# Performance work log

Hardware: AMD Instinct MI355X
Metric: run time of the kernel (lower is better)

## Reference

```python
import jax, jax.numpy as jnp
import numpy as np
from jax.scipy.linalg import solve_triangular

OMEGA0 = 30.0  # standard SIREN first-layer frequency


def setup_inputs() -> dict:
    key = jax.random.key(0)
    ks = jax.random.split(key, 12)
    B, NC, NT, XD, H, R = 64, 1024, 1024, 1, 512, 512
    x_context = jax.random.normal(ks[0], (B, NC, XD), jnp.float32)
    y_context = jax.random.normal(ks[1], (B, NC, 1), jnp.float32)
    x_target = jax.random.normal(ks[2], (B, NT, XD), jnp.float32)
    # SIREN MLP params (hidden_dims=[512,512,512], repr_dim=512)
    def lin(k, fi, fo, first=False):
        bound = 1.0 / fi if first else np.sqrt(6.0 / fi) / OMEGA0
        kW, kb = jax.random.split(k)
        W = jax.random.uniform(kW, (fi, fo), jnp.float32, -bound, bound)
        b = jax.random.uniform(kb, (fo,), jnp.float32, -bound, bound)
        return W, b
    W0, b0 = lin(ks[3], XD, H, first=True)
    W1, b1 = lin(ks[4], H, H)
    W2, b2 = lin(ks[5], H, H)
    Wr, br = lin(ks[6], H, R)
    log_noise_var = jnp.asarray(np.log(0.01), jnp.float32)
    return {"x_context": x_context, "y_context": y_context, "x_target": x_target,
            "W0": W0, "b0": b0, "W1": W1, "b1": b1, "W2": W2, "b2": b2,
            "Wr": Wr, "br": br, "log_noise_var": log_noise_var}


def _mlp(x, W0, b0, W1, b1, W2, b2, Wr, br):
    # SIREN: sine activations, omega_0 on first layer, linear head
    h = jnp.sin(OMEGA0 * (x @ W0 + b0))
    h = jnp.sin(h @ W1 + b1)
    h = jnp.sin(h @ W2 + b2)
    return h @ Wr + br


def reference(x_context, y_context, x_target, W0, b0, W1, b1, W2, b2, Wr, br, log_noise_var):
    mean = jnp.mean(y_context, axis=1, keepdims=True)          # [B,1,1]
    std = jnp.std(y_context, axis=1, keepdims=True, ddof=1)    # torch.std is unbiased
    yc = (y_context - mean) / std                              # [B,N,1]

    cr = _mlp(x_context, W0, b0, W1, b1, W2, b2, Wr, br)       # [B,N,R]
    tr = _mlp(x_target, W0, b0, W1, b1, W2, b2, Wr, br)        # [B,M,R]
    ones_c = jnp.ones(cr.shape[:-1] + (1,), cr.dtype)
    ones_t = jnp.ones(tr.shape[:-1] + (1,), tr.dtype)
    cr = jnp.concatenate([cr, ones_c], axis=-1)                # [B,N,R+1]
    tr = jnp.concatenate([tr, ones_t], axis=-1)                # [B,M,R+1]

    Rp1 = cr.shape[-1]
    cov = jnp.einsum('bnr,bns->brs', cr, cr)                   # [B,R+1,R+1]
    cov = cov + jnp.exp(log_noise_var) * jnp.eye(Rp1, dtype=cov.dtype)
    xty = jnp.einsum('bnr,bnd->brd', cr, yc)                   # [B,R+1,1]

    chol = jnp.linalg.cholesky(cov)                            # batched potrf
    z = solve_triangular(chol, xty, lower=True)
    w = solve_triangular(jnp.swapaxes(chol, -1, -2), z, lower=False)  # [B,R+1,1]

    y_pred = tr @ w                                            # [B,M,1]
    return y_pred * std + mean
```

## Files before the change

kernel.cpp:

```cpp
#include <hip/hip_runtime.h>
#include <hip/hip_fp16.h>
#include <math.h>

#define NB    64
#define NPTS  1024
#define HD    512
#define CPAD  576
#define COVE  ((size_t)NB*CPAD*CPAD)

typedef __attribute__((ext_vector_type(4))) float v4f;
typedef __attribute__((ext_vector_type(8))) short v8s;
typedef __attribute__((ext_vector_type(8))) _Float16 v8h;

__device__ __forceinline__ float sin_poly(float z){
  float t = z*z;
  float p = fmaf(t, -1.9841270e-4f, 8.3333333e-3f);
  p = fmaf(t, p, -0.16666667f);
  p = fmaf(t, p, 1.0f);
  return z*p;
}

__device__ __forceinline__ ushort2 split_f16(float a){
  _Float16 h = (_Float16)a;
  float hf = (float)h;
  _Float16 l = (_Float16)(a - hf);
  unsigned short uh, ul;
  __builtin_memcpy(&uh, &h, 2);
  __builtin_memcpy(&ul, &l, 2);
  ushort2 r; r.x = uh; r.y = ul;
  return r;
}

__device__ __forceinline__ unsigned short f16b(float a){
  _Float16 h = (_Float16)a;
  unsigned short uh; __builtin_memcpy(&uh, &h, 2);
  return uh;
}

__device__ __forceinline__ float f16r(float a){
  return (float)(_Float16)a;
}

__device__ __forceinline__ void g2l16(const unsigned short* g, unsigned short* l){
  __builtin_amdgcn_global_load_lds(
      (const __attribute__((address_space(1))) unsigned int*)(g),
      (__attribute__((address_space(3))) unsigned int*)(l), 16, 0, 0);
}

__global__ __launch_bounds__(256)
void prep_k(const float* __restrict__ W1, const float* __restrict__ W2,
            const float* __restrict__ Wr, unsigned short* __restrict__ wf,
            const float* __restrict__ y, float* __restrict__ meanv,
            float* __restrict__ stdv, float* __restrict__ ycb)
{
  __shared__ unsigned short tile[64][65];
  __shared__ float rs[4], rss[4], bc[2];
  const int tid = threadIdx.x;
  if (blockIdx.x >= 192){
    const int b = blockIdx.x - 192;
    const float* yb = y + (size_t)b*NPTS;
    float4 v = *(const float4*)(yb + tid*4);
    float s  = v.x+v.y+v.z+v.w;
    float ss = v.x*v.x+v.y*v.y+v.z*v.z+v.w*v.w;
    #pragma unroll
    for (int off=32; off; off>>=1){ s += __shfl_down(s, off); ss += __shfl_down(ss, off); }
    int wid = tid>>6, lane = tid&63;
    if (lane == 0){ rs[wid]=s; rss[wid]=ss; }
    __syncthreads();
    if (tid == 0){
      float S  = rs[0]+rs[1]+rs[2]+rs[3];
      float SS = rss[0]+rss[1]+rss[2]+rss[3];
      float mean = S * (1.0f/NPTS);
      float var  = (SS - S*S*(1.0f/NPTS)) * (1.0f/(NPTS-1));
      float sd = sqrtf(var);
      meanv[b]=mean; stdv[b]=sd; bc[0]=mean; bc[1]=1.0f/sd;
    }
    __syncthreads();
    float mean=bc[0], inv=bc[1];
    float4 o;
    o.x=(v.x-mean)*inv; o.y=(v.y-mean)*inv; o.z=(v.z-mean)*inv; o.w=(v.w-mean)*inv;
    *(float4*)(ycb + (size_t)b*NPTS + tid*4) = o;
    return;
  }
  const int mat = blockIdx.x >> 6;
  const int t = blockIdx.x & 63;
  const int k0 = (t >> 3)*64, n0 = (t & 7)*64;
  const float* W = (mat==0) ? W1 : ((mat==1) ? W2 : Wr);
  for (int idx=tid; idx<4096; idx+=256){
    int r = idx >> 6, c = idx & 63;
    tile[r][c] = f16b(W[(size_t)(k0+r)*512 + n0 + c]);
  }
  __syncthreads();
  unsigned short* dst = wf + (size_t)mat*262144;
  for (int idx=tid; idx<4096; idx+=256){
    int r = idx >> 6, c = idx & 63;
    dst[(size_t)(n0+r)*512 + k0 + c] = tile[c][r];
  }
}

__device__ __forceinline__ void h0c(const float* __restrict__ w0,
                                    const float* __restrict__ b0, int K0, int sq,
                                    float xv0, float xv1, v8s& pa0, v8s& pa1)
{
  const float* wp = w0 + K0 + sq*8;
  const float* bp = b0 + K0 + sq*8;
  float4 wva = *(const float4*)wp, wvb = *(const float4*)(wp+4);
  float4 bva = *(const float4*)bp, bvb = *(const float4*)(bp+4);
  float w8[8] = {wva.x,wva.y,wva.z,wva.w,wvb.x,wvb.y,wvb.z,wvb.w};
  float b8[8] = {bva.x,bva.y,bva.z,bva.w,bvb.x,bvb.y,bvb.z,bvb.w};
  #pragma unroll
  for (int i=0;i<8;++i){
    pa0[i] = (short)f16b(__sinf(30.f*fmaf(xv0, w8[i], b8[i])));
    pa1[i] = (short)f16b(__sinf(30.f*fmaf(xv1, w8[i], b8[i])));
  }
}

template<int EPI, int TRANS, int AMODE>
__global__ __launch_bounds__(256, 2)
void gemm_ld(const unsigned short* __restrict__ Ap,
             const float* __restrict__ xsrc, const float* __restrict__ w0,
             const float* __restrict__ b0,
             const unsigned short* __restrict__ Bw,
             const float* __restrict__ bias,
             unsigned short* __restrict__ Chi, unsigned short* __restrict__ Clo,
             const float* __restrict__ vvp, float* __restrict__ ydot, int rowBase)
{
  __shared__ unsigned short Ah[2][4096], Bh[2][8192];
  const int tid  = threadIdx.x;
  const int lane = tid & 63, wave = tid >> 6;
  const int wm = wave & 1, wn = wave >> 1;
  const int m0 = blockIdx.x*128, n0 = blockIdx.y*256;
  const int q = lane >> 4, ln16 = lane & 15;
  const int sr = tid >> 2, sq = tid & 3;
  const int qx  = (q ^ ((ln16>>1)&3))*8;
  const int swc = ((lane&3) ^ ((lane>>3)&3))*8;
  const int wsl = (sq ^ ((sr>>1)&3))*8;

  const int strowA = wave*32 + (lane>>2);
  const int strowB = wave*64 + (lane>>2);
  const unsigned short* gA = Ap + (size_t)(m0 + strowA)*512 + swc;
  const unsigned short* gB = Bw + (size_t)(n0 + strowB)*512 + swc;

  float xv0 = 0.f, xv1 = 0.f;
  if (AMODE == 1){ xv0 = xsrc[m0 + sr]; xv1 = xsrc[m0 + sr + 64]; }

  v4f acc[4][8];
  #pragma unroll
  for (int a=0;a<4;++a)
    #pragma unroll
    for (int b=0;b<8;++b) acc[a][b] = (v4f)(0.0f);

  v8s pa0, pa1;
  if (AMODE == 0){
    g2l16(gA, Ah[0]+wave*1024); g2l16(gA+16*512, Ah[0]+wave*1024+512);
  } else {
    h0c(w0, b0, 0, sq, xv0, xv1, pa0, pa1);
    *(v8s*)(Ah[0] + sr*32 + wsl) = pa0;
    *(v8s*)(Ah[0] + (sr+64)*32 + wsl) = pa1;
  }
  #pragma unroll
  for (int m=0;m<4;++m) g2l16(gB + m*16*512, Bh[0]+wave*2048 + m*512);
  __syncthreads();

  int cur = 0;
  for (int ks=0; ks<16; ++ks){
    const int nxt = cur^1;
    if (ks < 15){
      const int k1 = (ks+1)*32;
      if (AMODE == 0){
        g2l16(gA+k1, Ah[nxt]+wave*1024); g2l16(gA+k1+16*512, Ah[nxt]+wave*1024+512);
      }
      #pragma unroll
      for (int m=0;m<4;++m) g2l16(gB + k1 + m*16*512, Bh[nxt]+wave*2048 + m*512);
    }
    v8h bhf[8];
    #pragma unroll
    for (int nt=0; nt<8; ++nt){
      const int nrow = wn*128 + nt*16 + ln16;
      bhf[nt] = *(const v8h*)(Bh[cur] + nrow*32 + qx);
    }
    #pragma unroll
    for (int mt=0; mt<4; ++mt){
      const int mrow = wm*64 + mt*16 + ln16;
      v8h ah = *(const v8h*)(Ah[cur] + mrow*32 + qx);
      #pragma unroll
      for (int nt=0; nt<8; ++nt)
        acc[mt][nt] = __builtin_amdgcn_mfma_f32_16x16x32_f16(ah, bhf[nt], acc[mt][nt], 0,0,0);
    }
    if (AMODE == 1 && ks < 15){
      h0c(w0, b0, (ks+1)*32, sq, xv0, xv1, pa0, pa1);
      *(v8s*)(Ah[nxt] + sr*32 + wsl) = pa0;
      *(v8s*)(Ah[nxt] + (sr+64)*32 + wsl) = pa1;
    }
    __syncthreads();
    cur = nxt;
  }

  if (TRANS == 0){
    #pragma unroll
    for (int nt=0;nt<8;++nt){
      const int col = n0 + wn*128 + nt*16 + ln16;
      const float bl_ = bias[col];
      #pragma unroll
      for (int mt=0;mt<4;++mt){
        const int row0 = m0 + wm*64 + mt*16 + q*4;
        #pragma unroll
        for (int r=0;r<4;++r){
          float v = acc[mt][nt][r] + bl_;
          if (EPI == 1) v = sin_poly(v);
          Chi[(size_t)(row0+r)*512 + col] = f16b(v);
        }
      }
    }
  } else if (TRANS == 1){
    const int lb = m0 >> 10;
    #pragma unroll
    for (int nt=0;nt<8;++nt){
      const int col = n0 + wn*128 + nt*16 + ln16;
      const float bl_ = bias[col];
      #pragma unroll
      for (int mt=0;mt<4;++mt){
        const int row0 = m0 + wm*64 + mt*16 + q*4;
        const int nb = row0 & 1023;
        ushort4 h,l; ushort2 s;
        s=split_f16(acc[mt][nt][0]+bl_); h.x=s.x; l.x=s.y;
        s=split_f16(acc[mt][nt][1]+bl_); h.y=s.x; l.y=s.y;
        s=split_f16(acc[mt][nt][2]+bl_); h.z=s.x; l.z=s.y;
        s=split_f16(acc[mt][nt][3]+bl_); h.w=s.x; l.w=s.y;
        size_t o = ((size_t)lb*512 + col)*1024 + nb;
        *(ushort4*)(Chi + o) = h;
        *(ushort4*)(Clo + o) = l;
      }
    }
  } else {
    const int b = (rowBase + m0) >> 10;
    const float* vb = vvp + (size_t)b*512;
    float vcol[8];
    float bl_[8];
    #pragma unroll
    for (int nt=0;nt<8;++nt){
      const int col = n0 + wn*128 + nt*16 + ln16;
      vcol[nt] = vb[col];
      bl_[nt] = bias[col];
    }
    #pragma unroll
    for (int mt=0;mt<4;++mt){
      #pragma unroll
      for (int r=0;r<4;++r){
        float part = 0.f;
        #pragma unroll
        for (int nt=0;nt<8;++nt)
          part = fmaf(sin_poly(acc[mt][nt][r] + bl_[nt]), vcol[nt], part);
        #pragma unroll
        for (int off=1; off<16; off<<=1) part += __shfl_xor(part, off, 64);
        if (ln16 == 0){
          const int row = m0 + wm*64 + mt*16 + q*4 + r;
          atomicAdd(&ydot[rowBase + row], part);
        }
      }
    }
  }
}

__device__ __forceinline__ void ld_ext_row(const unsigned short* __restrict__ h,
                                           const unsigned short* __restrict__ l,
                                           const float* __restrict__ ycn,
                                           int f, int nofs, v8s& oh, v8s& ol)
{
  if (f < 512){
    oh = *(const v8s*)(h + (size_t)f*1024 + nofs);
    ol = *(const v8s*)(l + (size_t)f*1024 + nofs);
  } else if (f == 512){
    #pragma unroll
    for (int j=0;j<8;++j){ oh[j] = (short)0x3C00; ol[j] = 0; }
  } else if (f == 513){
    #pragma unroll
    for (int j=0;j<8;++j){
      ushort2 s = split_f16(ycn[nofs+j]);
      oh[j] = (short)s.x; ol[j] = (short)s.y;
    }
  } else {
    #pragma unroll
    for (int j=0;j<8;++j){ oh[j] = 0; ol[j] = 0; }
  }
}

__global__ __launch_bounds__(256)
void cov_ld(const unsigned short* __restrict__ CThi, const unsigned short* __restrict__ CTlo,
            const float* __restrict__ ycb,
            const float* __restrict__ lnv, float* __restrict__ cov, int bStart)
{
  int t = blockIdx.y;
  int ti = 0;
  while ((ti+1)*(ti+2)/2 <= t) ++ti;
  int tj = t - ti*(ti+1)/2;
  const int i0 = ti*128, j0 = tj*128;
  const int lb = blockIdx.x;
  const int b  = bStart + lb;
  const unsigned short* srch = CThi + (size_t)lb*512*1024;
  const unsigned short* srcl = CTlo + (size_t)lb*512*1024;
  const float* ycn = ycb + (size_t)b*NPTS;
  float* covb = cov + (size_t)b*CPAD*CPAD;
  const float noise = expf(lnv[0]);
  const bool diag = (i0 == j0);
  const bool aReg = (i0 == 512);

  __shared__ unsigned short Ah[2][4096], Al[2][4096], Bh2[2][4096], Bl2[2][4096];
  const int tid = threadIdx.x;
  const int lane = tid & 63, wave = tid >> 6;
  const int wm = wave & 1, wn = wave >> 1;
  const int q = lane >> 4, ln16 = lane & 15;
  const int sr = tid >> 2, sq = tid & 3;
  const int qx  = (q ^ ((ln16>>1)&3))*8;
  const int swc = ((lane&3) ^ ((lane>>3)&3))*8;
  const int wsl = (sq ^ ((sr>>1)&3))*8;
  const bool skipW = diag && (wave == 2);

  const int strow = wave*32 + (lane>>2);
  const size_t gaOff = (size_t)(i0 + strow)*1024 + swc;
  const size_t gbOff = (size_t)(j0 + strow)*1024 + swc;
  const int wb = wave*1024;

  v4f acc[4][4];
  #pragma unroll
  for (int a=0;a<4;++a)
    #pragma unroll
    for (int c=0;c<4;++c) acc[a][c] = (v4f)(0.0f);

  if (!aReg){
    g2l16(srch + gaOff, Ah[0]+wb); g2l16(srch + gaOff + (size_t)16*1024, Ah[0]+wb+512);
    g2l16(srcl + gaOff, Al[0]+wb); g2l16(srcl + gaOff + (size_t)16*1024, Al[0]+wb+512);
  } else {
    v8s th, tl;
    ld_ext_row(srch, srcl, ycn, i0 + sr, sq*8, th, tl);
    *(v8s*)(Ah[0] + sr*32 + wsl) = th; *(v8s*)(Al[0] + sr*32 + wsl) = tl;
    ld_ext_row(srch, srcl, ycn, i0 + sr + 64, sq*8, th, tl);
    *(v8s*)(Ah[0] + (sr+64)*32 + wsl) = th; *(v8s*)(Al[0] + (sr+64)*32 + wsl) = tl;
  }
  if (!diag){
    g2l16(srch + gbOff, Bh2[0]+wb); g2l16(srch + gbOff + (size_t)16*1024, Bh2[0]+wb+512);
    g2l16(srcl + gbOff, Bl2[0]+wb); g2l16(srcl + gbOff + (size_t)16*1024, Bl2[0]+wb+512);
  }
  __syncthreads();

  int cur = 0;
  for (int ks=0; ks<32; ++ks){
    const int nxt = cur^1;
    if (ks < 31){
      const int k1 = (ks+1)*32;
      if (!aReg){
        g2l16(srch + gaOff + k1, Ah[nxt]+wb);
        g2l16(srch + gaOff + k1 + (size_t)16*1024, Ah[nxt]+wb+512);
        g2l16(srcl + gaOff + k1, Al[nxt]+wb);
        g2l16(srcl + gaOff + k1 + (size_t)16*1024, Al[nxt]+wb+512);
      }
      if (!diag){
        g2l16(srch + gbOff + k1, Bh2[nxt]+wb);
        g2l16(srch + gbOff + k1 + (size_t)16*1024, Bh2[nxt]+wb+512);
        g2l16(srcl + gbOff + k1, Bl2[nxt]+wb);
        g2l16(srcl + gbOff + k1 + (size_t)16*1024, Bl2[nxt]+wb+512);
      }
    }
    if (!skipW){
      const unsigned short* BhP = diag ? Ah[cur] : Bh2[cur];
      const unsigned short* BlP = diag ? Al[cur] : Bl2[cur];
      v8h bhf[4], blf[4];
      #pragma unroll
      for (int nt=0; nt<4; ++nt){
        const int nrow = wn*64 + nt*16 + ln16;
        bhf[nt] = *(const v8h*)(BhP + nrow*32 + qx);
        blf[nt] = *(const v8h*)(BlP + nrow*32 + qx);
      }
      #pragma unroll
      for (int mt=0; mt<4; ++mt){
        const int mrow = wm*64 + mt*16 + ln16;
        v8h ah = *(const v8h*)(Ah[cur] + mrow*32 + qx);
        v8h al = *(const v8h*)(Al[cur] + mrow*32 + qx);
        #pragma unroll
        for (int nt=0; nt<4; ++nt){
          acc[mt][nt] = __builtin_amdgcn_mfma_f32_16x16x32_f16(ah, bhf[nt], acc[mt][nt], 0,0,0);
          acc[mt][nt] = __builtin_amdgcn_mfma_f32_16x16x32_f16(ah, blf[nt], acc[mt][nt], 0,0,0);
          acc[mt][nt] = __builtin_amdgcn_mfma_f32_16x16x32_f16(al, bhf[nt], acc[mt][nt], 0,0,0);
        }
      }
    }
    if (aReg && ks < 31){
      const int n1 = (ks+1)*32 + sq*8;
      v8s th, tl;
      ld_ext_row(srch, srcl, ycn, i0 + sr, n1, th, tl);
      *(v8s*)(Ah[nxt] + sr*32 + wsl) = th; *(v8s*)(Al[nxt] + sr*32 + wsl) = tl;
      ld_ext_row(srch, srcl, ycn, i0 + sr + 64, n1, th, tl);
      *(v8s*)(Ah[nxt] + (sr+64)*32 + wsl) = th; *(v8s*)(Al[nxt] + (sr+64)*32 + wsl) = tl;
    }
    __syncthreads();
    cur = nxt;
  }
  #pragma unroll
  for (int nt=0;nt<4;++nt){
    const int gj = j0 + wn*64 + nt*16 + ln16;
    #pragma unroll
    for (int mt=0;mt<4;++mt){
      const int gi0 = i0 + wm*64 + mt*16 + q*4;
      #pragma unroll
      for (int r=0;r<4;++r){
        const int gi = gi0 + r;
        if (gj <= gi && gi < CPAD && gj < CPAD){
          float v = acc[mt][nt][r];
          if (gi == gj) v += (gi < 513) ? noise : 1.0f;
          covb[(size_t)gi*CPAD + gj] = v;
        }
      }
    }
  }
}

__global__ __launch_bounds__(256)
void chol_trsm_k(float* __restrict__ cov, float* __restrict__ dchol, int k)
{
  (void)dchol;
  float* Ab = cov + (size_t)blockIdx.x * CPAD * CPAD;
  const int o = k*64;
  const int row0 = o + 64 + blockIdx.y*128;
  const int nrows = min(128, CPAD - row0);
  __shared__ float Ds[64][65];
  __shared__ float As[128][65];
  __shared__ float invd[64];
  const int tid = threadIdx.x;

  for (int idx=tid; idx<nrows*16; idx+=256){
    int r = idx >> 4, c = (idx & 15)*4;
    float4 v = *(const float4*)(Ab + (size_t)(row0+r)*CPAD + o + c);
    As[r][c]=v.x; As[r][c+1]=v.y; As[r][c+2]=v.z; As[r][c+3]=v.w;
  }

  if (tid < 64){
    float a[64];
    const float* rowp = Ab + (size_t)(o+tid)*CPAD + o;
    #pragma unroll
    for (int c=0; c<64; c+=4){
      float4 v = *(const float4*)(rowp + c);
      a[c]   = (c   <= tid) ? v.x : 0.f;
      a[c+1] = (c+1 <= tid) ? v.y : 0.f;
      a[c+2] = (c+2 <= tid) ? v.z : 0.f;
      a[c+3] = (c+3 <= tid) ? v.w : 0.f;
    }
    #pragma unroll
    for (int j=0; j<63; ++j){
      float vj = a[j];
      float t = vj * (1.0f / __shfl(vj, j, 64));
      #pragma unroll
      for (int c=j+1; c<64; ++c)
        a[c] = fmaf(-t, __shfl(vj, c, 64), a[c]);
    }
    float myinv = 0.f;
    #pragma unroll
    for (int c=0; c<64; ++c){
      float ic = 1.0f / sqrtf(__shfl(a[c], c, 64));
      a[c] *= ic;
      myinv = (c == tid) ? ic : myinv;
    }
    invd[tid] = myinv;
    #pragma unroll
    for (int c=0; c<64; ++c) Ds[tid][c] = a[c];
  }
  __syncthreads();

  const int srow = tid - 64;
  if (srow >= 0 && srow < nrows){
    float x[64];
    #pragma unroll
    for (int c=0; c<64; ++c){
      float s0 = As[srow][c], s1 = 0.f, s2 = 0.f, s3 = 0.f;
      #pragma unroll
      for (int j=0; j+4<=c; j+=4){
        s0 = fmaf(-x[j],   Ds[c][j],   s0);
        s1 = fmaf(-x[j+1], Ds[c][j+1], s1);
        s2 = fmaf(-x[j+2], Ds[c][j+2], s2);
        s3 = fmaf(-x[j+3], Ds[c][j+3], s3);
      }
      #pragma unroll
      for (int j = c & ~3; j < c; ++j)
        s0 = fmaf(-x[j], Ds[c][j], s0);
      x[c] = ((s0+s1)+(s2+s3)) * invd[c];
    }
    #pragma unroll
    for (int c=0; c<64; ++c) As[srow][c] = x[c];
  } else if (blockIdx.y == 0 && tid >= 192){
    const int r = tid - 192;
    float y[64];
    #pragma unroll
    for (int c = 63; c >= 0; --c){
      float s0 = (c == r) ? 1.0f : 0.0f, s1 = 0.f, s2 = 0.f, s3 = 0.f;
      #pragma unroll
      for (int j = c+1; j+4 <= 64; j += 4){
        s0 = fmaf(-Ds[j][c],   y[j],   s0);
        s1 = fmaf(-Ds[j+1][c], y[j+1], s1);
        s2 = fmaf(-Ds[j+2][c], y[j+2], s2);
        s3 = fmaf(-Ds[j+3][c], y[j+3], s3);
      }
      #pragma unroll
      for (int j = c+1 + ((63-c) & ~3); j < 64; ++j)
        s0 = fmaf(-Ds[j][c], y[j], s0);
      y[c] = ((s0+s1)+(s2+s3)) * invd[c];
    }
    float* dst = Ab + (size_t)(o + r)*CPAD + 512;
    #pragma unroll
    for (int c = 0; c < 64; c += 4)
      *(float4*)(dst + c) = make_float4(y[c], y[c+1], y[c+2], y[c+3]);
  }
  __syncthreads();
  for (int idx=tid; idx<nrows*16; idx+=256){
    int r = idx >> 4, c = (idx & 15)*4;
    float4 v = make_float4(As[r][c], As[r][c+1], As[r][c+2], As[r][c+3]);
    *(float4*)(Ab + (size_t)(row0+r)*CPAD + o + c) = v;
  }
}

__global__ __launch_bounds__(256)
void chol_trail_k(float* __restrict__ cov, int k)
{
  float* Ab = cov + (size_t)blockIdx.y * CPAD * CPAD;
  int t = blockIdx.x;
  int bi = 0;
  while ((bi+1)*(bi+2)/2 <= t) ++bi;
  int bj = t - bi*(bi+1)/2;
  const int o = k*64;
  const int s0 = o + 64;
  const int I = s0 + bi*64, J = s0 + bj*64;
  const bool diag = (bi == bj);

  __shared__ unsigned short Pih[64*72], Pil[64*72], Pjh[64*72], Pjl[64*72];
  const int tid = threadIdx.x;
  const int lane = tid & 63, wave = tid >> 6;
  const int q = lane >> 4, ln16 = lane & 15;

  for (int idx=tid; idx<1024; idx+=256){
    int r = idx >> 4, c = (idx & 15)*4;
    float4 v = *(const float4*)(Ab + (size_t)(I+r)*CPAD + o + c);
    ushort4 hh, ll; ushort2 s;
    s=split_f16(v.x); hh.x=s.x; ll.x=s.y;
    s=split_f16(v.y); hh.y=s.x; ll.y=s.y;
    s=split_f16(v.z); hh.z=s.x; ll.z=s.y;
    s=split_f16(v.w); hh.w=s.x; ll.w=s.y;
    *(ushort4*)(Pih + r*72 + c) = hh;
    *(ushort4*)(Pil + r*72 + c) = ll;
    if (!diag){
      float4 u = *(const float4*)(Ab + (size_t)(J+r)*CPAD + o + c);
      s=split_f16(u.x); hh.x=s.x; ll.x=s.y;
      s=split_f16(u.y); hh.y=s.x; ll.y=s.y;
      s=split_f16(u.z); hh.z=s.x; ll.z=s.y;
      s=split_f16(u.w); hh.w=s.x; ll.w=s.y;
      *(ushort4*)(Pjh + r*72 + c) = hh;
      *(ushort4*)(Pjl + r*72 + c) = ll;
    }
  }
  __syncthreads();
  const unsigned short* Bh = diag ? Pih : Pjh;
  const unsigned short* Bl = diag ? Pil : Pjl;

  v4f acc[4];
  #pragma unroll
  for (int nt=0;nt<4;++nt) acc[nt] = (v4f)(0.0f);

  #pragma unroll
  for (int ks=0; ks<2; ++ks){
    const int ko = ks*32 + q*8;
    v8h ah = *(const v8h*)(Pih + (wave*16 + ln16)*72 + ko);
    v8h al = *(const v8h*)(Pil + (wave*16 + ln16)*72 + ko);
    #pragma unroll
    for (int nt=0; nt<4; ++nt){
      v8h bh = *(const v8h*)(Bh + (nt*16 + ln16)*72 + ko);
      v8h bl = *(const v8h*)(Bl + (nt*16 + ln16)*72 + ko);
      acc[nt] = __builtin_amdgcn_mfma_f32_16x16x32_f16(ah, bh, acc[nt], 0,0,0);
      acc[nt] = __builtin_amdgcn_mfma_f32_16x16x32_f16(ah, bl, acc[nt], 0,0,0);
      acc[nt] = __builtin_amdgcn_mfma_f32_16x16x32_f16(al, bh, acc[nt], 0,0,0);
    }
  }

  #pragma unroll
  for (int nt=0; nt<4; ++nt){
    const int gj = J + nt*16 + ln16;
    #pragma unroll
    for (int r=0; r<4; ++r){
      const int gi = I + wave*16 + q*4 + r;
      if (gj <= gi)
        Ab[(size_t)gi*CPAD + gj] -= acc[nt][r];
    }
  }
}

__global__ __launch_bounds__(256)
void chol_last_k(float* __restrict__ cov, float* __restrict__ dchol)
{
  float* Ab = cov + (size_t)blockIdx.x * CPAD * CPAD;
  __shared__ float P[64][65];
  __shared__ float Ds[64][65];
  __shared__ float invl[64];
  const int tid = threadIdx.x;

  for (int idx=tid; idx<1024; idx+=256){
    int r = idx >> 4, c = (idx & 15)*4;
    float4 v = *(const float4*)(Ab + (size_t)(512+r)*CPAD + 448 + c);
    P[r][c]=v.x; P[r][c+1]=v.y; P[r][c+2]=v.z; P[r][c+3]=v.w;
    float4 u = *(const float4*)(Ab + (size_t)(512+r)*CPAD + 512 + c);
    Ds[r][c]   = (c   <= r) ? u.x : 0.f;
    Ds[r][c+1] = (c+1 <= r) ? u.y : 0.f;
    Ds[r][c+2] = (c+2 <= r) ? u.z : 0.f;
    Ds[r][c+3] = (c+3 <= r) ? u.w : 0.f;
  }
  __syncthreads();
  {
    const int tx = tid & 15, ty = tid >> 4;
    float acc[4][4];
    #pragma unroll
    for (int r=0;r<4;++r)
      #pragma unroll
      for (int c=0;c<4;++c) acc[r][c]=0.f;
    for (int kk=0; kk<64; ++kk){
      float av[4], bv[4];
      #pragma unroll
      for (int r=0;r<4;++r) av[r] = P[tx*4+r][kk];
      #pragma unroll
      for (int c=0;c<4;++c) bv[c] = P[ty*4+c][kk];
      #pragma unroll
      for (int r=0;r<4;++r)
        #pragma unroll
        for (int c=0;c<4;++c) acc[r][c] = fmaf(av[r], bv[c], acc[r][c]);
    }
    __syncthreads();
    #pragma unroll
    for (int r=0;r<4;++r){
      int gi = tx*4 + r;
      #pragma unroll
      for (int c=0;c<4;++c){
        int gj = ty*4 + c;
        if (gj <= gi) Ds[gi][gj] -= acc[r][c];
      }
    }
  }
  __syncthreads();

  if (tid < 64){
    float a[64];
    #pragma unroll
    for (int c=0; c<64; ++c) a[c] = Ds[tid][c];
    #pragma unroll
    for (int j=0; j<63; ++j){
      float vj = a[j];
      float t = vj * (1.0f / __shfl(vj, j, 64));
      #pragma unroll
      for (int c=j+1; c<64; ++c)
        a[c] = fmaf(-t, __shfl(vj, c, 64), a[c]);
    }
    float myinv = 0.f;
    #pragma unroll
    for (int c=0; c<64; ++c){
      float ic = 1.0f / sqrtf(__shfl(a[c], c, 64));
      a[c] *= ic;
      myinv = (c == tid) ? ic : myinv;
    }
    invl[tid] = myinv;
    #pragma unroll
    for (int c=0; c<64; ++c) Ds[tid][c] = a[c];
  }
  __syncthreads();

  float* dst = dchol + ((size_t)blockIdx.x*9 + 8)*4096;
  for (int idx=tid; idx<4096; idx+=256)
    dst[idx] = Ds[idx>>6][idx&63];
  if (tid < 64){
    const int r = tid;
    float y[64];
    #pragma unroll
    for (int c = 63; c >= 0; --c){
      float s0 = (c == r) ? 1.0f : 0.0f, s1 = 0.f, s2 = 0.f, s3 = 0.f;
      #pragma unroll
      for (int j = c+1; j+4 <= 64; j += 4){
        s0 = fmaf(-Ds[j][c],   y[j],   s0);
        s1 = fmaf(-Ds[j+1][c], y[j+1], s1);
        s2 = fmaf(-Ds[j+2][c], y[j+2], s2);
        s3 = fmaf(-Ds[j+3][c], y[j+3], s3);
      }
      #pragma unroll
      for (int j = c+1 + ((63-c) & ~3); j < 64; ++j)
        s0 = fmaf(-Ds[j][c], y[j], s0);
      y[c] = ((s0+s1)+(s2+s3)) * invl[c];
    }
    float* dst2 = Ab + (size_t)(512 + r)*CPAD + 512;
    #pragma unroll
    for (int c = 0; c < 64; c += 4)
      *(float4*)(dst2 + c) = make_float4(y[c], y[c+1], y[c+2], y[c+3]);
  }
}

__global__ __launch_bounds__(1024)
void back_solve_k(const float* __restrict__ cov, const float* __restrict__ dchol,
                  const float* __restrict__ Wr, const float* __restrict__ br,
                  float* __restrict__ vv, float* __restrict__ cvec,
                  float* __restrict__ ydot)
{
  const int b = blockIdx.x;
  const float* L = cov + (size_t)b*CPAD*CPAD;
  const float* dc = dchol + (size_t)b*9*4096;
  __shared__ float inv2[64*64];
  __shared__ float rhs[CPAD];
  __shared__ float xv[64];
  __shared__ float red[4*512];
  const int tid = threadIdx.x;
  const int pr = tid >> 4, pc = (tid & 15)*4;
  const float* zrow = L + (size_t)513*CPAD;

  for (int i=tid; i<CPAD; i+=1024)
    rhs[i] = (i < 512) ? zrow[i] : ((i == 512) ? dc[8*4096 + 64] : 0.f);
  {
    float4 v = *(const float4*)(L + (size_t)(512 + pr)*CPAD + 512 + pc);
    *(float4*)(inv2 + pr*64 + pc) = v;
  }
  __syncthreads();

  for (int k=8; k>=1; --k){
    const int o = k*64;
    const int G = o >> 2;
    const int act = G << 2;
    float4 v16[16];
    int rg = 0, cg = 0;
    if (tid < act){
      rg = tid / G; cg = tid % G;
      const float* lp = L + (size_t)(o + rg*16)*CPAD + cg*4;
      #pragma unroll
      for (int rr=0; rr<16; ++rr)
        v16[rr] = *(const float4*)(lp + (size_t)rr*CPAD);
    }
    float4 pf = *(const float4*)(L + (size_t)((k-1)*64 + pr)*CPAD + 512 + pc);
    if (tid < 64){
      float acc = 0.f;
      #pragma unroll
      for (int j=0;j<64;++j) acc = fmaf(inv2[j*64 + tid], rhs[o+j], acc);
      xv[tid] = acc;
      rhs[o+tid] = acc;
    }
    __syncthreads();
    if (tid < act){
      float4 s = {0.f,0.f,0.f,0.f};
      #pragma unroll
      for (int rr=0; rr<16; ++rr){
        float xr = xv[rg*16 + rr];
        s.x = fmaf(v16[rr].x, xr, s.x);
        s.y = fmaf(v16[rr].y, xr, s.y);
        s.z = fmaf(v16[rr].z, xr, s.z);
        s.w = fmaf(v16[rr].w, xr, s.w);
      }
      *(float4*)(red + rg*512 + cg*4) = s;
    }
    __syncthreads();
    if (tid < o)
      rhs[tid] -= (red[tid] + red[512+tid]) + (red[1024+tid] + red[1536+tid]);
    *(float4*)(inv2 + pr*64 + pc) = pf;
    __syncthreads();
  }
  if (tid < 64){
    float acc = 0.f;
    #pragma unroll
    for (int j=0;j<64;++j) acc = fmaf(inv2[j*64 + tid], rhs[j], acc);
    rhs[tid] = acc;
  }
  __syncthreads();

  ydot[(size_t)b*1024 + tid] = 0.f;
  const int j = tid >> 1, h = tid & 1;
  {
    float acc = 0.f;
    const float* row = Wr + (size_t)j*512 + h*256;
    const float* wsp = rhs + h*256;
    for (int r=0; r<256; r+=4){
      float4 w4 = *(const float4*)(row + r);
      acc = fmaf(f16r(w4.x), wsp[r],   acc);
      acc = fmaf(f16r(w4.y), wsp[r+1], acc);
      acc = fmaf(f16r(w4.z), wsp[r+2], acc);
      acc = fmaf(f16r(w4.w), wsp[r+3], acc);
    }
    red[tid] = acc;
  }
  __syncthreads();
  if (h == 0) vv[(size_t)b*512 + j] = red[tid] + red[tid+1];
  __syncthreads();
  red[tid] = (tid < 512) ? br[tid]*rhs[tid] : 0.f;
  __syncthreads();
  for (int s2=512; s2>0; s2>>=1){
    if (tid < s2) red[tid] += red[tid+s2];
    __syncthreads();
  }
  if (tid == 0) cvec[b] = red[0] + rhs[512];
}

__global__ __launch_bounds__(256)
void fin_k(const float* __restrict__ ydot, const float* __restrict__ cvec,
           const float* __restrict__ meanv, const float* __restrict__ stdv,
           float* __restrict__ out)
{
  int i = blockIdx.x*256 + threadIdx.x;
  int b = i >> 10;
  out[i] = fmaf(ydot[i] + cvec[b], stdv[b], meanv[b]);
}

extern "C" void kernel_launch(void* const* d_in, const int* in_sizes, int n_in,
                              void* d_out, int out_size, void* d_ws, size_t ws_size,
                              hipStream_t stream)
{
  (void)in_sizes; (void)n_in; (void)out_size;
  const float* x_ctx = (const float*)d_in[0];
  const float* y_ctx = (const float*)d_in[1];
  const float* x_tgt = (const float*)d_in[2];
  const float* W0 = (const float*)d_in[3];
  const float* b0 = (const float*)d_in[4];
  const float* W1 = (const float*)d_in[5];
  const float* b1 = (const float*)d_in[6];
  const float* W2 = (const float*)d_in[7];
  const float* b2 = (const float*)d_in[8];
  const float* Wr = (const float*)d_in[9];
  const float* br = (const float*)d_in[10];
  const float* lnv = (const float*)d_in[11];
  float* out = (float*)d_out;
  float* ws = (float*)d_ws;

  int CH = 65536;
  for (;;){
    size_t fl = COVE + 65536 + 192 + (size_t)64*512 + (size_t)64*CPAD + 65536
              + (size_t)64*9*4096 + 64;
    size_t sh = (size_t)3*262144 + (size_t)2*CH*512 + (size_t)2*(CH/1024)*512*1024;
    size_t need = fl*4 + sh*2;
    if (ws_size >= need || CH <= 1024) break;
    CH >>= 1;
  }
  const int nch = 65536 / CH;
  const int bpc = CH / NPTS;

  float* cov   = ws;
  float* ycb   = cov + COVE;
  float* meanv = ycb + 65536;
  float* stdv  = meanv + 64;
  float* cvec  = stdv + 64;
  float* vvb   = cvec + 64;
  float* wvb   = vvb + (size_t)64*512;
  float* ydot  = wvb + (size_t)64*CPAD;
  float* dchol = ydot + 65536;
  unsigned short* wf   = (unsigned short*)(dchol + (size_t)64*9*4096);
  unsigned short* P0   = wf + (size_t)3*262144;
  unsigned short* P1   = P0 + (size_t)CH*512;
  unsigned short* CThi = P1 + (size_t)CH*512;
  unsigned short* CTlo = CThi + (size_t)bpc*512*1024;

  prep_k<<<256, 256, 0, stream>>>(W1, W2, Wr, wf, y_ctx, meanv, stdv, ycb);

  for (int c=0; c<nch; ++c){
    const float* xc = x_ctx + (size_t)c*CH;
    dim3 g(CH/128, 2);
    gemm_ld<1,0,1><<<g, 256, 0, stream>>>(0, xc, W0, b0, wf, b1, P1, 0, 0, 0, 0);
    gemm_ld<1,0,0><<<g, 256, 0, stream>>>(P1, 0, 0, 0, wf+262144, b2, P0, 0, 0, 0, 0);
    gemm_ld<0,1,0><<<g, 256, 0, stream>>>(P0, 0, 0, 0, wf+524288, br, CThi, CTlo, 0, 0, 0);
    cov_ld<<<dim3(bpc, 15), 256, 0, stream>>>(CThi, CTlo, ycb, lnv, cov, c*bpc);
  }

  for (int k=0; k<8; ++k){
    const int cnt = CPAD - k*64 - 64;
    chol_trsm_k<<<dim3(NB, (cnt + 127)/128), 256, 0, stream>>>(cov, dchol, k);
    if (k < 7){
      const int tcnt = cnt >> 6;
      chol_trail_k<<<dim3(tcnt*(tcnt+1)/2, NB), 256, 0, stream>>>(cov, k);
    }
  }
  chol_last_k<<<NB, 256, 0, stream>>>(cov, dchol);
  back_solve_k<<<NB, 1024, 0, stream>>>(cov, dchol, Wr, br, vvb, cvec, ydot);

  for (int c=0; c<nch; ++c){
    const float* xt = x_tgt + (size_t)c*CH;
    dim3 g(CH/128, 2);
    gemm_ld<1,0,1><<<g, 256, 0, stream>>>(0, xt, W0, b0, wf, b1, P1, 0, 0, 0, 0);
    gemm_ld<1,2,0><<<g, 256, 0, stream>>>(P1, 0, 0, 0, wf+262144, b2, 0, 0, vvb, ydot, c*CH);
  }
  fin_k<<<256, 256, 0, stream>>>(ydot, cvec, meanv, stdv, out);
}
```

Measured before the change: 1.075 ms.

## Fuse next diagonal-block factorization into trailing update and use MFMA TRSM

The first tile of each trailing-update launch now factors the next 64x64 diagonal block in place and stores its inverse lower factor into the padding columns. The following panel solve becomes a split-fp16 MFMA multiply by that stored inverse, replacing the sequential per-row substitution in chol_trsm_k. The intent is to take the serial diagonal factorization and triangular solve off the critical path of each Cholesky step. In exchange, one block per batch carries a long single-wave serial section, and multiplying by an explicit inverse in split precision may change accuracy.

```diff
diff --git a/kernel.cpp b/kernel.cpp
--- a/kernel.cpp
+++ b/kernel.cpp
@@ -517,6 +517,81 @@
 }
 
 __global__ __launch_bounds__(256)
+void chol_trsmM_k(float* __restrict__ cov, int k)
+{
+  float* Ab = cov + (size_t)blockIdx.x * CPAD * CPAD;
+  const int o = k*64;
+  const int row0 = o + 64 + blockIdx.y*128;
+  const int nrows = min(128, CPAD - row0);
+  __shared__ unsigned short Mh[64*72], Ml[64*72], Ph[128*72], Pl[128*72];
+  const int tid = threadIdx.x;
+  const int lane = tid & 63, wave = tid >> 6;
+  const int q = lane >> 4, ln16 = lane & 15;
+
+  for (int idx=tid; idx<1024; idx+=256){
+    int r = idx >> 4, c = (idx & 15)*4;
+    float4 v = *(const float4*)(Ab + (size_t)(o+r)*CPAD + 512 + c);
+    ushort4 hh, ll; ushort2 s;
+    s=split_f16(v.x); hh.x=s.x; ll.x=s.y;
+    s=split_f16(v.y); hh.y=s.x; ll.y=s.y;
+    s=split_f16(v.z); hh.z=s.x; ll.z=s.y;
+    s=split_f16(v.w); hh.w=s.x; ll.w=s.y;
+    *(ushort4*)(Mh + r*72 + c) = hh;
+    *(ushort4*)(Ml + r*72 + c) = ll;
+  }
+  for (int idx=tid; idx<nrows*16; idx+=256){
+    int r = idx >> 4, c = (idx & 15)*4;
+    float4 v = *(const float4*)(Ab + (size_t)(row0+r)*CPAD + o + c);
+    ushort4 hh, ll; ushort2 s;
+    s=split_f16(v.x); hh.x=s.x; ll.x=s.y;
+    s=split_f16(v.y); hh.y=s.x; ll.y=s.y;
+    s=split_f16(v.z); hh.z=s.x; ll.z=s.y;
+    s=split_f16(v.w); hh.w=s.x; ll.w=s.y;
+    *(ushort4*)(Ph + r*72 + c) = hh;
+    *(ushort4*)(Pl + r*72 + c) = ll;
+  }
+  __syncthreads();
+
+  v4f acc[2][4];
+  #pragma unroll
+  for (int rt=0;rt<2;++rt)
+    #pragma unroll
+    for (int nt=0;nt<4;++nt) acc[rt][nt] = (v4f)(0.0f);
+
+  #pragma unroll
+  for (int ks=0; ks<2; ++ks){
+    const int ko = ks*32 + q*8;
+    #pragma unroll
+    for (int rt=0; rt<2; ++rt){
+      const int ar = wave*32 + rt*16 + ln16;
+      v8h ah = *(const v8h*)(Ph + ar*72 + ko);
+      v8h al = *(const v8h*)(Pl + ar*72 + ko);
+      #pragma unroll
+      for (int nt=0; nt<4; ++nt){
+        v8h bh = *(const v8h*)(Mh + (nt*16 + ln16)*72 + ko);
+        v8h bl = *(const v8h*)(Ml + (nt*16 + ln16)*72 + ko);
+        acc[rt][nt] = __builtin_amdgcn_mfma_f32_16x16x32_f16(ah, bh, acc[rt][nt], 0,0,0);
+        acc[rt][nt] = __builtin_amdgcn_mfma_f32_16x16x32_f16(ah, bl, acc[rt][nt], 0,0,0);
+        acc[rt][nt] = __builtin_amdgcn_mfma_f32_16x16x32_f16(al, bh, acc[rt][nt], 0,0,0);
+      }
+    }
+  }
+
+  #pragma unroll
+  for (int rt=0; rt<2; ++rt){
+    #pragma unroll
+    for (int nt=0; nt<4; ++nt){
+      #pragma unroll
+      for (int r=0; r<4; ++r){
+        const int lr = wave*32 + rt*16 + q*4 + r;
+        if (lr < nrows)
+          Ab[(size_t)(row0+lr)*CPAD + o + nt*16 + ln16] = acc[rt][nt][r];
+      }
+    }
+  }
+}
+
+__global__ __launch_bounds__(256)
 void chol_trail_k(float* __restrict__ cov, int k)
 {
   float* Ab = cov + (size_t)blockIdx.y * CPAD * CPAD;
@@ -528,8 +603,14 @@
   const int s0 = o + 64;
   const int I = s0 + bi*64, J = s0 + bj*64;
   const bool diag = (bi == bj);
-
-  __shared__ unsigned short Pih[64*72], Pil[64*72], Pjh[64*72], Pjl[64*72];
+  const bool term = (bi == 0) && (bj == 0);
+
+  __shared__ unsigned short Pih[64*72], Pil[64*72];
+  __shared__ __align__(16) unsigned short PjBuf[2][64*72];
+  __shared__ float invl[64];
+  unsigned short* Pjh = PjBuf[0];
+  unsigned short* Pjl = PjBuf[1];
+  float* Ds = (float*)PjBuf;
   const int tid = threadIdx.x;
   const int lane = tid & 63, wave = tid >> 6;
   const int q = lane >> 4, ln16 = lane & 15;
@@ -577,14 +658,76 @@
     }
   }
 
-  #pragma unroll
-  for (int nt=0; nt<4; ++nt){
-    const int gj = J + nt*16 + ln16;
-    #pragma unroll
-    for (int r=0; r<4; ++r){
-      const int gi = I + wave*16 + q*4 + r;
-      if (gj <= gi)
-        Ab[(size_t)gi*CPAD + gj] -= acc[nt][r];
+  if (!term){
+    #pragma unroll
+    for (int nt=0; nt<4; ++nt){
+      const int gj = J + nt*16 + ln16;
+      #pragma unroll
+      for (int r=0; r<4; ++r){
+        const int gi = I + wave*16 + q*4 + r;
+        if (gj <= gi)
+          Ab[(size_t)gi*CPAD + gj] -= acc[nt][r];
+      }
+    }
+  } else {
+    __syncthreads();
+    #pragma unroll
+    for (int nt=0; nt<4; ++nt){
+      const int lj = nt*16 + ln16;
+      #pragma unroll
+      for (int r=0; r<4; ++r){
+        const int li = wave*16 + q*4 + r;
+        float u = (lj <= li) ? (Ab[(size_t)(I+li)*CPAD + J+lj] - acc[nt][r]) : 0.f;
+        Ds[li*66 + lj] = u;
+      }
+    }
+    __syncthreads();
+    if (tid < 64){
+      float a[64];
+      #pragma unroll
+      for (int c=0;c<64;++c) a[c] = Ds[tid*66 + c];
+      #pragma unroll
+      for (int j=0;j<63;++j){
+        float vj = a[j];
+        float tt = vj * (1.0f/__shfl(vj, j, 64));
+        #pragma unroll
+        for (int c=j+1;c<64;++c)
+          a[c] = fmaf(-tt, __shfl(vj, c, 64), a[c]);
+      }
+      float myinv = 0.f;
+      #pragma unroll
+      for (int c=0;c<64;++c){
+        float ic = 1.0f/sqrtf(__shfl(a[c], c, 64));
+        a[c] *= ic;
+        myinv = (c==tid) ? ic : myinv;
+      }
+      invl[tid] = myinv;
+      #pragma unroll
+      for (int c=0;c<64;++c) Ds[tid*66 + c] = a[c];
+    }
+    __syncthreads();
+    if (tid < 64){
+      const int r = tid;
+      float y[64];
+      #pragma unroll
+      for (int c=63;c>=0;--c){
+        float s0 = (c==r)?1.f:0.f, s1=0.f, s2=0.f, s3=0.f;
+        #pragma unroll
+        for (int j=c+1;j+4<=64;j+=4){
+          s0 = fmaf(-Ds[j*66+c],     y[j],   s0);
+          s1 = fmaf(-Ds[(j+1)*66+c], y[j+1], s1);
+          s2 = fmaf(-Ds[(j+2)*66+c], y[j+2], s2);
+          s3 = fmaf(-Ds[(j+3)*66+c], y[j+3], s3);
+        }
+        #pragma unroll
+        for (int j=c+1+((63-c)&~3); j<64; ++j)
+          s0 = fmaf(-Ds[j*66+c], y[j], s0);
+        y[c] = ((s0+s1)+(s2+s3)) * invl[c];
+      }
+      float* dst = Ab + (size_t)(I + r)*CPAD + 512;
+      #pragma unroll
+      for (int c=0;c<64;c+=4)
+        *(float4*)(dst + c) = make_float4(y[c], y[c+1], y[c+2], y[c+3]);
     }
   }
 }
@@ -861,13 +1004,16 @@
     cov_ld<<<dim3(bpc, 15), 256, 0, stream>>>(CThi, CTlo, ycb, lnv, cov, c*bpc);
   }
 
-  for (int k=0; k<8; ++k){
-    const int cnt = CPAD - k*64 - 64;
-    chol_trsm_k<<<dim3(NB, (cnt + 127)/128), 256, 0, stream>>>(cov, dchol, k);
-    if (k < 7){
+  {
+    chol_trsm_k<<<dim3(NB, 4), 256, 0, stream>>>(cov, dchol, 0);
+    chol_trail_k<<<dim3(36, NB), 256, 0, stream>>>(cov, 0);
+    for (int k=1; k<7; ++k){
+      const int cnt = CPAD - k*64 - 64;
+      chol_trsmM_k<<<dim3(NB, (cnt + 127)/128), 256, 0, stream>>>(cov, k);
       const int tcnt = cnt >> 6;
       chol_trail_k<<<dim3(tcnt*(tcnt+1)/2, NB), 256, 0, stream>>>(cov, k);
     }
+    chol_trsmM_k<<<dim3(NB, 1), 256, 0, stream>>>(cov, 7);
   }
   chol_last_k<<<NB, 256, 0, stream>>>(cov, dchol);
   back_solve_k<<<NB, 1024, 0, stream>>>(cov, dchol, Wr, br, vvb, cvec, ydot);
```

Result: slower. 1.248 ms (+16.1%).

## Split Cholesky panel into factor kernel and MFMA-based TRSM via inverse multiply

Applied to the files above, without the earlier changes.

Splits the per-panel step into a small kernel that factors the 64x64 diagonal block and writes its inverse, and a second kernel that solves the panel rows by multiplying with that inverse using split-fp16 MFMA. This replaces the serial per-row forward substitution with matrix-core work. The cost is one extra launch per panel and a numerical risk from explicit inversion combined with three-term fp16 splitting.

```diff
diff --git a/kernel.cpp b/kernel.cpp
--- a/kernel.cpp
+++ b/kernel.cpp
@@ -414,105 +414,140 @@
   }
 }
 
+__global__ __launch_bounds__(64)
+void chol_fact_k(float* __restrict__ cov, int k)
+{
+  float* Ab = cov + (size_t)blockIdx.x * CPAD * CPAD;
+  const int o = k*64;
+  __shared__ float Ds[64][65];
+  __shared__ float invd[64];
+  const int tid = threadIdx.x;
+
+  float a[64];
+  const float* rowp = Ab + (size_t)(o+tid)*CPAD + o;
+  #pragma unroll
+  for (int c=0; c<64; c+=4){
+    float4 v = *(const float4*)(rowp + c);
+    a[c]   = (c   <= tid) ? v.x : 0.f;
+    a[c+1] = (c+1 <= tid) ? v.y : 0.f;
+    a[c+2] = (c+2 <= tid) ? v.z : 0.f;
+    a[c+3] = (c+3 <= tid) ? v.w : 0.f;
+  }
+  #pragma unroll
+  for (int j=0; j<63; ++j){
+    float vj = a[j];
+    float t = vj * (1.0f / __shfl(vj, j, 64));
+    #pragma unroll
+    for (int c=j+1; c<64; ++c)
+      a[c] = fmaf(-t, __shfl(vj, c, 64), a[c]);
+  }
+  float myinv = 0.f;
+  #pragma unroll
+  for (int c=0; c<64; ++c){
+    float ic = 1.0f / sqrtf(__shfl(a[c], c, 64));
+    a[c] *= ic;
+    myinv = (c == tid) ? ic : myinv;
+  }
+  invd[tid] = myinv;
+  #pragma unroll
+  for (int c=0; c<64; ++c) Ds[tid][c] = a[c];
+  __syncthreads();
+
+  const int r = tid;
+  float y[64];
+  #pragma unroll
+  for (int c = 63; c >= 0; --c){
+    float s0 = (c == r) ? 1.0f : 0.0f, s1 = 0.f, s2 = 0.f, s3 = 0.f;
+    #pragma unroll
+    for (int j = c+1; j+4 <= 64; j += 4){
+      s0 = fmaf(-Ds[j][c],   y[j],   s0);
+      s1 = fmaf(-Ds[j+1][c], y[j+1], s1);
+      s2 = fmaf(-Ds[j+2][c], y[j+2], s2);
+      s3 = fmaf(-Ds[j+3][c], y[j+3], s3);
+    }
+    #pragma unroll
+    for (int j = c+1 + ((63-c) & ~3); j < 64; ++j)
+      s0 = fmaf(-Ds[j][c], y[j], s0);
+    y[c] = ((s0+s1)+(s2+s3)) * invd[c];
+  }
+  float* dst = Ab + (size_t)(o + r)*CPAD + 512;
+  #pragma unroll
+  for (int c = 0; c < 64; c += 4)
+    *(float4*)(dst + c) = make_float4(y[c], y[c+1], y[c+2], y[c+3]);
+}
+
 __global__ __launch_bounds__(256)
-void chol_trsm_k(float* __restrict__ cov, float* __restrict__ dchol, int k)
-{
-  (void)dchol;
+void chol_trsmM_k(float* __restrict__ cov, int k)
+{
   float* Ab = cov + (size_t)blockIdx.x * CPAD * CPAD;
   const int o = k*64;
   const int row0 = o + 64 + blockIdx.y*128;
   const int nrows = min(128, CPAD - row0);
-  __shared__ float Ds[64][65];
-  __shared__ float As[128][65];
-  __shared__ float invd[64];
+  __shared__ unsigned short Mh[64*72], Ml[64*72], Ph[128*72], Pl[128*72];
   const int tid = threadIdx.x;
-
+  const int lane = tid & 63, wave = tid >> 6;
+  const int q = lane >> 4, ln16 = lane & 15;
+
+  for (int idx=tid; idx<1024; idx+=256){
+    int r = idx >> 4, c = (idx & 15)*4;
+    float4 v = *(const float4*)(Ab + (size_t)(o+r)*CPAD + 512 + c);
+    ushort4 hh, ll; ushort2 s;
+    s=split_f16(v.x); hh.x=s.x; ll.x=s.y;
+    s=split_f16(v.y); hh.y=s.x; ll.y=s.y;
+    s=split_f16(v.z); hh.z=s.x; ll.z=s.y;
+    s=split_f16(v.w); hh.w=s.x; ll.w=s.y;
+    *(ushort4*)(Mh + r*72 + c) = hh;
+    *(ushort4*)(Ml + r*72 + c) = ll;
+  }
   for (int idx=tid; idx<nrows*16; idx+=256){
     int r = idx >> 4, c = (idx & 15)*4;
     float4 v = *(const float4*)(Ab + (size_t)(row0+r)*CPAD + o + c);
-    As[r][c]=v.x; As[r][c+1]=v.y; As[r][c+2]=v.z; As[r][c+3]=v.w;
-  }
-
-  if (tid < 64){
-    float a[64];
-    const float* rowp = Ab + (size_t)(o+tid)*CPAD + o;
-    #pragma unroll
-    for (int c=0; c<64; c+=4){
-      float4 v = *(const float4*)(rowp + c);
-      a[c]   = (c   <= tid) ? v.x : 0.f;
-      a[c+1] = (c+1 <= tid) ? v.y : 0.f;
-      a[c+2] = (c+2 <= tid) ? v.z : 0.f;
-      a[c+3] = (c+3 <= tid) ? v.w : 0.f;
-    }
-    #pragma unroll
-    for (int j=0; j<63; ++j){
-      float vj = a[j];
-      float t = vj * (1.0f / __shfl(vj, j, 64));
-      #pragma unroll
-      for (int c=j+1; c<64; ++c)
-        a[c] = fmaf(-t, __shfl(vj, c, 64), a[c]);
-    }
-    float myinv = 0.f;
-    #pragma unroll
-    for (int c=0; c<64; ++c){
-      float ic = 1.0f / sqrtf(__shfl(a[c], c, 64));
-      a[c] *= ic;
-      myinv = (c == tid) ? ic : myinv;
-    }
-    invd[tid] = myinv;
-    #pragma unroll
-    for (int c=0; c<64; ++c) Ds[tid][c] = a[c];
-  }
-  __syncthreads();
-
-  const int srow = tid - 64;
-  if (srow >= 0 && srow < nrows){
-    float x[64];
-    #pragma unroll
-    for (int c=0; c<64; ++c){
-      float s0 = As[srow][c], s1 = 0.f, s2 = 0.f, s3 = 0.f;
-      #pragma unroll
-      for (int j=0; j+4<=c; j+=4){
-        s0 = fmaf(-x[j],   Ds[c][j],   s0);
-        s1 = fmaf(-x[j+1], Ds[c][j+1], s1);
-        s2 = fmaf(-x[j+2], Ds[c][j+2], s2);
-        s3 = fmaf(-x[j+3], Ds[c][j+3], s3);
-      }
-      #pragma unroll
-      for (int j = c & ~3; j < c; ++j)
-        s0 = fmaf(-x[j], Ds[c][j], s0);
-      x[c] = ((s0+s1)+(s2+s3)) * invd[c];
-    }
-    #pragma unroll
-    for (int c=0; c<64; ++c) As[srow][c] = x[c];
-  } else if (blockIdx.y == 0 && tid >= 192){
-    const int r = tid - 192;
-    float y[64];
-    #pragma unroll
-    for (int c = 63; c >= 0; --c){
-      float s0 = (c == r) ? 1.0f : 0.0f, s1 = 0.f, s2 = 0.f, s3 = 0.f;
-      #pragma unroll
-      for (int j = c+1; j+4 <= 64; j += 4){
-        s0 = fmaf(-Ds[j][c],   y[j],   s0);
-        s1 = fmaf(-Ds[j+1][c], y[j+1], s1);
-        s2 = fmaf(-Ds[j+2][c], y[j+2], s2);
-        s3 = fmaf(-Ds[j+3][c], y[j+3], s3);
-      }
-      #pragma unroll
-      for (int j = c+1 + ((63-c) & ~3); j < 64; ++j)
-        s0 = fmaf(-Ds[j][c], y[j], s0);
-      y[c] = ((s0+s1)+(s2+s3)) * invd[c];
-    }
-    float* dst = Ab + (size_t)(o + r)*CPAD + 512;
-    #pragma unroll
-    for (int c = 0; c < 64; c += 4)
-      *(float4*)(dst + c) = make_float4(y[c], y[c+1], y[c+2], y[c+3]);
-  }
-  __syncthreads();
-  for (int idx=tid; idx<nrows*16; idx+=256){
-    int r = idx >> 4, c = (idx & 15)*4;
-    float4 v = make_float4(As[r][c], As[r][c+1], As[r][c+2], As[r][c+3]);
-    *(float4*)(Ab + (size_t)(row0+r)*CPAD + o + c) = v;
+    ushort4 hh, ll; ushort2 s;
+    s=split_f16(v.x); hh.x=s.x; ll.x=s.y;
+    s=split_f16(v.y); hh.y=s.x; ll.y=s.y;
+    s=split_f16(v.z); hh.z=s.x; ll.z=s.y;
+    s=split_f16(v.w); hh.w=s.x; ll.w=s.y;
+    *(ushort4*)(Ph + r*72 + c) = hh;
+    *(ushort4*)(Pl + r*72 + c) = ll;
+  }
+  __syncthreads();
+
+  v4f acc[2][4];
+  #pragma unroll
+  for (int rt=0;rt<2;++rt)
+    #pragma unroll
+    for (int nt=0;nt<4;++nt) acc[rt][nt] = (v4f)(0.0f);
+
+  #pragma unroll
+  for (int ks=0; ks<2; ++ks){
+    const int ko = ks*32 + q*8;
+    #pragma unroll
+    for (int rt=0; rt<2; ++rt){
+      const int ar = wave*32 + rt*16 + ln16;
+      v8h ah = *(const v8h*)(Ph + ar*72 + ko);
+      v8h al = *(const v8h*)(Pl + ar*72 + ko);
+      #pragma unroll
+      for (int nt=0; nt<4; ++nt){
+        v8h bh = *(const v8h*)(Mh + (nt*16 + ln16)*72 + ko);
+        v8h bl = *(const v8h*)(Ml + (nt*16 + ln16)*72 + ko);
+        acc[rt][nt] = __builtin_amdgcn_mfma_f32_16x16x32_f16(ah, bh, acc[rt][nt], 0,0,0);
+        acc[rt][nt] = __builtin_amdgcn_mfma_f32_16x16x32_f16(ah, bl, acc[rt][nt], 0,0,0);
+        acc[rt][nt] = __builtin_amdgcn_mfma_f32_16x16x32_f16(al, bh, acc[rt][nt], 0,0,0);
+      }
+    }
+  }
+
+  #pragma unroll
+  for (int rt=0; rt<2; ++rt){
+    #pragma unroll
+    for (int nt=0; nt<4; ++nt){
+      #pragma unroll
+      for (int r=0; r<4; ++r){
+        const int lr = wave*32 + rt*16 + q*4 + r;
+        if (lr < nrows)
+          Ab[(size_t)(row0+lr)*CPAD + o + nt*16 + ln16] = acc[rt][nt][r];
+      }
+    }
   }
 }
 
@@ -861,12 +896,15 @@
     cov_ld<<<dim3(bpc, 15), 256, 0, stream>>>(CThi, CTlo, ycb, lnv, cov, c*bpc);
   }
 
-  for (int k=0; k<8; ++k){
-    const int cnt = CPAD - k*64 - 64;
-    chol_trsm_k<<<dim3(NB, (cnt + 127)/128), 256, 0, stream>>>(cov, dchol, k);
-    if (k < 7){
-      const int tcnt = cnt >> 6;
+  {
+    chol_fact_k<<<NB, 64, 0, stream>>>(cov, 0);
+    chol_trsmM_k<<<dim3(NB, 4), 256, 0, stream>>>(cov, 0);
+    for (int k=0; k<7; ++k){
+      const int tcnt = (CPAD - k*64 - 64) >> 6;
       chol_trail_k<<<dim3(tcnt*(tcnt+1)/2, NB), 256, 0, stream>>>(cov, k);
+      chol_fact_k<<<NB, 64, 0, stream>>>(cov, k+1);
+      const int cnt2 = CPAD - (k+1)*64 - 64;
+      chol_trsmM_k<<<dim3(NB, (cnt2 + 127)/128), 256, 0, stream>>>(cov, k+1);
     }
   }
   chol_last_k<<<NB, 256, 0, stream>>>(cov, dchol);
```

After: 1.778 ms. +65.4%, slower.
